# Kernel tuning notes

Measured on AMD Instinct MI355X. Metric: run time of the kernel, lower is better.

## Reference

```python
import jax, jax.numpy as jnp
import numpy as np
import math

SCALE = 30.0
OUT_INDICATOR = 1.0  # easy_margin=False -> out_indicator = 1


def setup_inputs() -> dict:
    key = jax.random.key(0)
    k1, k2, k3 = jax.random.split(key, 3)
    B, D, C = 1024, 512, 100000
    feat = jax.random.normal(k1, (B, D), dtype=jnp.float32)
    label = jax.random.randint(k2, (B,), 0, C, dtype=jnp.int64)
    # xavier_uniform_ init for weights [C, D]
    limit = math.sqrt(6.0 / (C + D))
    weights = jax.random.uniform(k3, (C, D), dtype=jnp.float32, minval=-limit, maxval=limit)
    return {"feat": feat, "label": label, "weights": weights}


def reference(feat, label, weights):
    # L2-normalize features and class weights
    norm_f = jnp.linalg.norm(feat, axis=-1, keepdims=True)        # [B,1]
    nf = feat / norm_f
    norm_w = jnp.linalg.norm(weights, axis=-1, keepdims=True)     # [C,1]
    nw = weights / norm_w
    cos = nf @ nw.T                                               # [B,C]

    avg_w_norm = jnp.mean(norm_w)
    avg_x_norm = jnp.mean(norm_f)

    B = feat.shape[0]
    idx = jnp.arange(B)
    target_cos = jnp.clip(cos[idx, label], -1.0, 1.0)             # [B]
    thetas = jnp.arccos(target_cos) / jnp.pi * 180.0              # degrees, [B]

    max_theta = jnp.max(thetas)
    min_theta = jnp.min(thetas)
    avg_theta = jnp.mean(thetas)
    stdv_theta = jnp.std(thetas, ddof=1)                          # sample stddev (n-1)

    # per-sample dynamic margin (radians). In the torch code these are Python
    # floats computed via .item(), hence constants w.r.t. autograd.
    margin_above = jnp.where(max_theta < 90.0, (90.0 - avg_theta) / 180.0 * jnp.pi, 0.0)
    margin_below = min_theta / 180.0 * jnp.pi
    the_margin = jnp.where(thetas > avg_theta, margin_above, margin_below)  # [B]

    in_range = target_cos > -jnp.cos(the_margin)
    margin_add = jnp.where(in_range, the_margin, 0.0)
    margin_ext = jnp.where(in_range, 0.0, -the_margin * jnp.sin(the_margin)) * OUT_INDICATOR
    margin_add = jax.lax.stop_gradient(margin_add)
    margin_ext = jax.lax.stop_gradient(margin_ext)

    # cos(acos(cos) + margin) only differs from cos at target positions
    target_marginal = jnp.cos(jnp.arccos(target_cos) + margin_add) + margin_ext  # [B]
    marginal_logits = SCALE * cos.at[idx, label].set(target_marginal)            # [B,C]

    return (cos, marginal_logits, avg_theta, min_theta, max_theta,
            stdv_theta, avg_w_norm, avg_x_norm)
```

## Files before the change

kernel.cpp:

```cpp
#include <hip/hip_runtime.h>
#include <math.h>
#include <stdint.h>


typedef _Float16 f16x8 __attribute__((ext_vector_type(8)));
typedef float f32x4 __attribute__((ext_vector_type(4)));

#define SCALE_S 30.0f
#define RAD2DEG 57.29577951308232f
#define DEG2RAD 0.017453292519943295f

#define GL16(g, l)                                                    \
  __builtin_amdgcn_global_load_lds(                                   \
      (const __attribute__((address_space(1))) void*)(g),             \
      (__attribute__((address_space(3))) void*)(l), 16, 0, 0)

__global__ __launch_bounds__(64) void norm_cvt_kernel(
    const float* __restrict__ X, _Float16* __restrict__ X16, int K, int Cn,
    float* __restrict__ nrm, float* __restrict__ inv) {
  const int row = blockIdx.x;
  const int t = threadIdx.x;
  _Float16* o = X16 + (size_t)row * K;
  if (row >= Cn) {
    for (int k = t * 8; k < K; k += 64 * 8)
      *(f16x8*)(o + k) = (f16x8)(_Float16)0.f;
    return;
  }
  const float* r = X + (size_t)row * K;
  float s = 0.f;
  for (int k = t * 8; k < K; k += 64 * 8) {
    float4 v0 = *(const float4*)(r + k);
    float4 v1 = *(const float4*)(r + k + 4);
    s += v0.x * v0.x + v0.y * v0.y + v0.z * v0.z + v0.w * v0.w +
         v1.x * v1.x + v1.y * v1.y + v1.z * v1.z + v1.w * v1.w;
    f16x8 h;
    h[0] = (_Float16)v0.x; h[1] = (_Float16)v0.y;
    h[2] = (_Float16)v0.z; h[3] = (_Float16)v0.w;
    h[4] = (_Float16)v1.x; h[5] = (_Float16)v1.y;
    h[6] = (_Float16)v1.z; h[7] = (_Float16)v1.w;
    *(f16x8*)(o + k) = h;
  }
#pragma unroll
  for (int off = 32; off > 0; off >>= 1) s += __shfl_down(s, off);
  if (t == 0) {
    float n = sqrtf(s);
    nrm[row] = n;
    inv[row] = 1.0f / n;
  }
}

__global__ __launch_bounds__(64) void row_norms_kernel(
    const float* __restrict__ X, int K,
    float* __restrict__ nrm, float* __restrict__ inv) {
  const int row = blockIdx.x;
  const float* r = X + (size_t)row * K;
  const int t = threadIdx.x;
  float s = 0.f;
  for (int k = t * 4; k < K; k += 64 * 4) {
    float4 v = *(const float4*)(r + k);
    s += v.x * v.x + v.y * v.y + v.z * v.z + v.w * v.w;
  }
#pragma unroll
  for (int off = 32; off > 0; off >>= 1) s += __shfl_down(s, off);
  if (t == 0) {
    float n = sqrtf(s);
    nrm[row] = n;
    inv[row] = 1.0f / n;
  }
}

__global__ __launch_bounds__(256) void gemm_cos_lds(
    const _Float16* __restrict__ A16, const _Float16* __restrict__ W16,
    const float* __restrict__ inv_nf, const float* __restrict__ inv_nw,
    float* __restrict__ cosO, float* __restrict__ margO,
    int Cn, int npanel) {
  __shared__ __align__(16) _Float16 Ash[128 * 64];
  __shared__ __align__(16) _Float16 Wsh[128 * 64];
  const int K = 512;

  const int nblk = npanel * 8;
  const int lin = blockIdx.x;
  const int q = nblk >> 3;
  const int wg = (lin & 7) * q + (lin >> 3);
  const int bm = (wg & 7) * 128;
  const int bn = (wg >> 3) * 128;

  const int t = threadIdx.x;
  const int lane = t & 63;
  const int w = t >> 6;
  const int wm = (w >> 1) * 64;
  const int wn = (w & 1) * 64;
  const int lrow = lane >> 4;
  const int lcol = lane & 15;

  const _Float16* srcA[4];
  const _Float16* srcW[4];
  _Float16* dstA[4];
  _Float16* dstW[4];
#pragma unroll
  for (int i = 0; i < 4; ++i) {
    const int slot = w * 4 + i;
    const int c = slot * 64 + lane;
    const int row = c >> 3;
    const int kc = (c & 7) ^ (row & 7);
    srcA[i] = A16 + (size_t)(bm + row) * K + kc * 8;
    srcW[i] = W16 + (size_t)(bn + row) * K + kc * 8;
    dstA[i] = Ash + slot * 512;
    dstW[i] = Wsh + slot * 512;
  }

  f32x4 acc[4][4];
#pragma unroll
  for (int m = 0; m < 4; ++m)
#pragma unroll
    for (int n = 0; n < 4; ++n) acc[m][n] = (f32x4)0.f;

  for (int s = 0; s < 8; ++s) {
    __syncthreads();
#pragma unroll
    for (int i = 0; i < 4; ++i) {
      GL16(srcA[i], dstA[i]);
      GL16(srcW[i], dstW[i]);
      srcA[i] += 64;
      srcW[i] += 64;
    }
    __syncthreads();

#pragma unroll
    for (int ks = 0; ks < 2; ++ks) {
      f16x8 af[4], bf[4];
      const int kc = ks * 4 + lrow;
#pragma unroll
      for (int m = 0; m < 4; ++m) {
        const int rowa = wm + m * 16 + lcol;
        af[m] = *(const f16x8*)(Ash + rowa * 64 + ((kc ^ (rowa & 7)) * 8));
        const int rowb = wn + m * 16 + lcol;
        bf[m] = *(const f16x8*)(Wsh + rowb * 64 + ((kc ^ (rowb & 7)) * 8));
      }
#pragma unroll
      for (int m = 0; m < 4; ++m)
#pragma unroll
        for (int n = 0; n < 4; ++n)
          acc[m][n] = __builtin_amdgcn_mfma_f32_16x16x32_f16(
              af[m], bf[n], acc[m][n], 0, 0, 0);
    }
  }

  float fi[4][4];
#pragma unroll
  for (int m = 0; m < 4; ++m)
#pragma unroll
    for (int r = 0; r < 4; ++r)
      fi[m][r] = inv_nf[bm + wm + m * 16 + lrow * 4 + r];

#pragma unroll
  for (int n = 0; n < 4; ++n) {
    const int col = bn + wn + n * 16 + lcol;
    if (col < Cn) {
      const float wiv = inv_nw[col];
#pragma unroll
      for (int m = 0; m < 4; ++m) {
        const int row0 = bm + wm + m * 16 + lrow * 4;
#pragma unroll
        for (int r = 0; r < 4; ++r) {
          const float v = acc[m][n][r] * fi[m][r] * wiv;
          const size_t o = (size_t)(row0 + r) * Cn + col;
          __builtin_nontemporal_store(v, cosO + o);
          __builtin_nontemporal_store(SCALE_S * v, margO + o);
        }
      }
    }
  }
}

__global__ __launch_bounds__(256) void gemm_cos_f16(
    const float* __restrict__ A, const float* __restrict__ W,
    const float* __restrict__ inv_nf, const float* __restrict__ inv_nw,
    float* __restrict__ cosO, float* __restrict__ margO,
    int Cn, int K, int npanel) {
  __shared__ __align__(16) _Float16 Ash[128 * 64];
  __shared__ __align__(16) _Float16 Wsh[128 * 64];

  const int nblk = npanel * 8;
  const int lin = blockIdx.x;
  const int q = nblk >> 3;
  const int wg = (lin & 7) * q + (lin >> 3);
  const int bm = (wg & 7) * 128;
  const int bn = (wg >> 3) * 128;

  const int t = threadIdx.x;
  const int lane = t & 63;
  const int wid = t >> 6;
  const int wm = (wid >> 1) * 64;
  const int wn = (wid & 1) * 64;
  const int lrow = lane >> 4;
  const int lcol = lane & 15;

  int srow[4], skc[4];
#pragma unroll
  for (int j = 0; j < 4; ++j) {
    const int c = t + 256 * j;
    srow[j] = c >> 3;
    skc[j] = (t & 7) ^ (srow[j] & 7);
  }

  f32x4 acc[4][4];
#pragma unroll
  for (int m = 0; m < 4; ++m)
#pragma unroll
    for (int n = 0; n < 4; ++n) acc[m][n] = (f32x4)0.f;

  float4 ra[4][2], rw[4][2];
#pragma unroll
  for (int j = 0; j < 4; ++j) {
    const float* ap = A + (size_t)(bm + srow[j]) * K + skc[j] * 8;
    ra[j][0] = *(const float4*)ap;
    ra[j][1] = *(const float4*)(ap + 4);
    const int wr = bn + srow[j];
    if (wr < Cn) {
      const float* wp = W + (size_t)wr * K + skc[j] * 8;
      rw[j][0] = *(const float4*)wp;
      rw[j][1] = *(const float4*)(wp + 4);
    } else {
      rw[j][0] = make_float4(0.f, 0.f, 0.f, 0.f);
      rw[j][1] = make_float4(0.f, 0.f, 0.f, 0.f);
    }
  }

  const int nstep = K / 64;
  for (int s = 0; s < nstep; ++s) {
    __syncthreads();
#pragma unroll
    for (int j = 0; j < 4; ++j) {
      const int c = t + 256 * j;
      f16x8 ha, hw;
#pragma unroll
      for (int qq = 0; qq < 4; ++qq) {
        ha[qq] = (_Float16)((&ra[j][0].x)[qq]);
        ha[4 + qq] = (_Float16)((&ra[j][1].x)[qq]);
        hw[qq] = (_Float16)((&rw[j][0].x)[qq]);
        hw[4 + qq] = (_Float16)((&rw[j][1].x)[qq]);
      }
      *(f16x8*)(Ash + c * 8) = ha;
      *(f16x8*)(Wsh + c * 8) = hw;
    }
    __syncthreads();

    if (s + 1 < nstep) {
      const int k0 = (s + 1) * 64;
#pragma unroll
      for (int j = 0; j < 4; ++j) {
        const float* ap = A + (size_t)(bm + srow[j]) * K + k0 + skc[j] * 8;
        ra[j][0] = *(const float4*)ap;
        ra[j][1] = *(const float4*)(ap + 4);
        const int wr = bn + srow[j];
        if (wr < Cn) {
          const float* wp = W + (size_t)wr * K + k0 + skc[j] * 8;
          rw[j][0] = *(const float4*)wp;
          rw[j][1] = *(const float4*)(wp + 4);
        } else {
          rw[j][0] = make_float4(0.f, 0.f, 0.f, 0.f);
          rw[j][1] = make_float4(0.f, 0.f, 0.f, 0.f);
        }
      }
    }

#pragma unroll
    for (int ks = 0; ks < 2; ++ks) {
      f16x8 af[4], bf[4];
      const int kc = ks * 4 + lrow;
#pragma unroll
      for (int m = 0; m < 4; ++m) {
        const int rowa = wm + m * 16 + lcol;
        af[m] = *(const f16x8*)(Ash + rowa * 64 + ((kc ^ (rowa & 7)) * 8));
        const int rowb = wn + m * 16 + lcol;
        bf[m] = *(const f16x8*)(Wsh + rowb * 64 + ((kc ^ (rowb & 7)) * 8));
      }
#pragma unroll
      for (int m = 0; m < 4; ++m)
#pragma unroll
        for (int n = 0; n < 4; ++n)
          acc[m][n] = __builtin_amdgcn_mfma_f32_16x16x32_f16(
              af[m], bf[n], acc[m][n], 0, 0, 0);
    }
  }

  float fi[4][4];
#pragma unroll
  for (int m = 0; m < 4; ++m)
#pragma unroll
    for (int r = 0; r < 4; ++r)
      fi[m][r] = inv_nf[bm + wm + m * 16 + lrow * 4 + r];

#pragma unroll
  for (int n = 0; n < 4; ++n) {
    const int col = bn + wn + n * 16 + lcol;
    if (col < Cn) {
      const float wiv = inv_nw[col];
#pragma unroll
      for (int m = 0; m < 4; ++m) {
        const int row0 = bm + wm + m * 16 + lrow * 4;
#pragma unroll
        for (int r = 0; r < 4; ++r) {
          const float v = acc[m][n][r] * fi[m][r] * wiv;
          const size_t o = (size_t)(row0 + r) * Cn + col;
          __builtin_nontemporal_store(v, cosO + o);
          __builtin_nontemporal_store(SCALE_S * v, margO + o);
        }
      }
    }
  }
}

__global__ __launch_bounds__(1024) void stats_fixup_kernel(
    const float* __restrict__ cosO, float* __restrict__ margO,
    const int* __restrict__ label,
    const float* __restrict__ norm_f, const float* __restrict__ norm_w,
    float* __restrict__ scal, int B, int Cn, int Wn) {
  __shared__ float red[1024];
  __shared__ float s_stat[4];
  const int t = threadIdx.x;

  const int lb = label[t];
  float tc = cosO[(size_t)t * Cn + lb];
  tc = fminf(1.0f, fmaxf(-1.0f, tc));
  const float theta = acosf(tc) * RAD2DEG;

  red[t] = theta; __syncthreads();
  for (int s = 512; s > 0; s >>= 1) {
    if (t < s) red[t] += red[t + s];
    __syncthreads();
  }
  if (t == 0) s_stat[2] = red[0] / (float)B;
  __syncthreads();
  const float avg = s_stat[2];
  __syncthreads();

  red[t] = theta; __syncthreads();
  for (int s = 512; s > 0; s >>= 1) {
    if (t < s) red[t] = fmaxf(red[t], red[t + s]);
    __syncthreads();
  }
  if (t == 0) s_stat[0] = red[0];
  __syncthreads();
  const float mx = s_stat[0];
  __syncthreads();

  red[t] = theta; __syncthreads();
  for (int s = 512; s > 0; s >>= 1) {
    if (t < s) red[t] = fminf(red[t], red[t + s]);
    __syncthreads();
  }
  if (t == 0) s_stat[1] = red[0];
  __syncthreads();
  const float mn = s_stat[1];
  __syncthreads();

  {
    const float d = theta - avg;
    red[t] = d * d;
  }
  __syncthreads();
  for (int s = 512; s > 0; s >>= 1) {
    if (t < s) red[t] += red[t + s];
    __syncthreads();
  }
  const float stdv = sqrtf(red[0] / (float)(B - 1));
  __syncthreads();

  const float margin_above = (mx < 90.0f) ? (90.0f - avg) * DEG2RAD : 0.0f;
  const float margin_below = mn * DEG2RAD;
  const float the_margin = (theta > avg) ? margin_above : margin_below;
  const bool in_range = tc > -cosf(the_margin);
  const float margin_add = in_range ? the_margin : 0.0f;
  const float margin_ext = in_range ? 0.0f : -the_margin * sinf(the_margin);
  const float tmarg = cosf(acosf(tc) + margin_add) + margin_ext;
  margO[(size_t)t * Cn + lb] = SCALE_S * tmarg;

  float pw = 0.f;
  for (int i = t; i < Wn; i += 1024) pw += norm_w[i];
  red[t] = pw; __syncthreads();
  for (int s = 512; s > 0; s >>= 1) {
    if (t < s) red[t] += red[t + s];
    __syncthreads();
  }
  const float avg_w = red[0] / (float)Wn;
  __syncthreads();

  red[t] = norm_f[t]; __syncthreads();
  for (int s = 512; s > 0; s >>= 1) {
    if (t < s) red[t] += red[t + s];
    __syncthreads();
  }
  const float avg_x = red[0] / (float)B;

  if (t == 0) {
    scal[0] = avg;
    scal[1] = mn;
    scal[2] = mx;
    scal[3] = stdv;
    scal[4] = avg_w;
    scal[5] = avg_x;
  }
}

extern "C" void kernel_launch(void* const* d_in, const int* in_sizes, int n_in,
                              void* d_out, int out_size, void* d_ws, size_t ws_size,
                              hipStream_t stream) {
  const float* feat = (const float*)d_in[0];
  const int* label = (const int*)d_in[1];
  const float* W = (const float*)d_in[2];

  const int B = in_sizes[1];
  const int K = in_sizes[0] / B;
  const int Cn = in_sizes[2] / K;
  const int CnPad = ((Cn + 127) / 128) * 128;
  const int npanel = CnPad / 128;

  float* cosO = (float*)d_out;
  float* margO = cosO + (size_t)B * Cn;
  float* scal = margO + (size_t)B * Cn;

  float* norm_f = (float*)d_ws;
  float* inv_nf = norm_f + B;
  float* norm_w = inv_nf + B;
  float* inv_nw = norm_w + CnPad;
  _Float16* A16 = (_Float16*)(inv_nw + CnPad);
  _Float16* W16 = A16 + (size_t)B * K;

  const size_t need = sizeof(float) * (2 * (size_t)B + 2 * (size_t)CnPad) +
                      sizeof(_Float16) * ((size_t)B * K + (size_t)CnPad * K);

  if (ws_size >= need) {
    norm_cvt_kernel<<<B, 64, 0, stream>>>(feat, A16, K, B, norm_f, inv_nf);
    norm_cvt_kernel<<<CnPad, 64, 0, stream>>>(W, W16, K, Cn, norm_w, inv_nw);
    gemm_cos_lds<<<npanel * 8, 256, 0, stream>>>(A16, W16, inv_nf, inv_nw,
                                                 cosO, margO, Cn, npanel);
  } else {
    row_norms_kernel<<<B, 64, 0, stream>>>(feat, K, norm_f, inv_nf);
    row_norms_kernel<<<Cn, 64, 0, stream>>>(W, K, norm_w, inv_nw);
    gemm_cos_f16<<<npanel * 8, 256, 0, stream>>>(feat, W, inv_nf, inv_nw,
                                                 cosO, margO, Cn, K, npanel);
  }

  stats_fixup_kernel<<<1, B, 0, stream>>>(cosO, margO, label, norm_f, norm_w,
                                          scal, B, Cn, Cn);
}
```

Measured before the change: 371.7 us.

## Double-buffer GEMM LDS tiles and pack four rows per norm-convert block

The GEMM now keeps two LDS buffers for the A and W tiles. It prefetches the next K-slab with global_load_lds while computing on the current one, which drops one barrier per iteration and overlaps load latency with MFMA work. The norm/convert kernel now handles four rows per 256-thread block and uses nontemporal loads and stores to avoid polluting the cache with the streamed weights. Double buffering doubles LDS use per block, which may reduce occupancy, and the fast path now also requires K to be a multiple of 512.

```diff
diff --git a/kernel.cpp b/kernel.cpp
--- a/kernel.cpp
+++ b/kernel.cpp
@@ -15,22 +15,31 @@
       (const __attribute__((address_space(1))) void*)(g),             \
       (__attribute__((address_space(3))) void*)(l), 16, 0, 0)
 
-__global__ __launch_bounds__(64) void norm_cvt_kernel(
+__global__ __launch_bounds__(256) void norm_cvt4(
     const float* __restrict__ X, _Float16* __restrict__ X16, int K, int Cn,
-    float* __restrict__ nrm, float* __restrict__ inv) {
-  const int row = blockIdx.x;
-  const int t = threadIdx.x;
+    float* __restrict__ nrm, float* __restrict__ inv, int rows) {
+  const int wid = threadIdx.x >> 6;
+  const int lane = threadIdx.x & 63;
+  const int row = blockIdx.x * 4 + wid;
+  if (row >= rows) return;
   _Float16* o = X16 + (size_t)row * K;
   if (row >= Cn) {
-    for (int k = t * 8; k < K; k += 64 * 8)
-      *(f16x8*)(o + k) = (f16x8)(_Float16)0.f;
+    for (int k = lane * 8; k < K; k += 512)
+      __builtin_nontemporal_store((f16x8)(_Float16)0.f, (f16x8*)(o + k));
     return;
   }
   const float* r = X + (size_t)row * K;
   float s = 0.f;
-  for (int k = t * 8; k < K; k += 64 * 8) {
-    float4 v0 = *(const float4*)(r + k);
-    float4 v1 = *(const float4*)(r + k + 4);
+  for (int k = lane * 8; k < K; k += 512) {
+    float4 v0, v1;
+    v0.x = __builtin_nontemporal_load(r + k + 0);
+    v0.y = __builtin_nontemporal_load(r + k + 1);
+    v0.z = __builtin_nontemporal_load(r + k + 2);
+    v0.w = __builtin_nontemporal_load(r + k + 3);
+    v1.x = __builtin_nontemporal_load(r + k + 4);
+    v1.y = __builtin_nontemporal_load(r + k + 5);
+    v1.z = __builtin_nontemporal_load(r + k + 6);
+    v1.w = __builtin_nontemporal_load(r + k + 7);
     s += v0.x * v0.x + v0.y * v0.y + v0.z * v0.z + v0.w * v0.w +
          v1.x * v1.x + v1.y * v1.y + v1.z * v1.z + v1.w * v1.w;
     f16x8 h;
@@ -38,11 +47,11 @@
     h[2] = (_Float16)v0.z; h[3] = (_Float16)v0.w;
     h[4] = (_Float16)v1.x; h[5] = (_Float16)v1.y;
     h[6] = (_Float16)v1.z; h[7] = (_Float16)v1.w;
-    *(f16x8*)(o + k) = h;
+    __builtin_nontemporal_store(h, (f16x8*)(o + k));
   }
 #pragma unroll
   for (int off = 32; off > 0; off >>= 1) s += __shfl_down(s, off);
-  if (t == 0) {
+  if (lane == 0) {
     float n = sqrtf(s);
     nrm[row] = n;
     inv[row] = 1.0f / n;
@@ -74,8 +83,8 @@
     const float* __restrict__ inv_nf, const float* __restrict__ inv_nw,
     float* __restrict__ cosO, float* __restrict__ margO,
     int Cn, int npanel) {
-  __shared__ __align__(16) _Float16 Ash[128 * 64];
-  __shared__ __align__(16) _Float16 Wsh[128 * 64];
+  __shared__ __align__(16) _Float16 Ash[2][128 * 64];
+  __shared__ __align__(16) _Float16 Wsh[2][128 * 64];
   const int K = 512;
 
   const int nblk = npanel * 8;
@@ -88,6 +97,7 @@
   const int t = threadIdx.x;
   const int lane = t & 63;
   const int w = t >> 6;
+  const int w4 = w * 4;
   const int wm = (w >> 1) * 64;
   const int wn = (w & 1) * 64;
   const int lrow = lane >> 4;
@@ -95,18 +105,13 @@
 
   const _Float16* srcA[4];
   const _Float16* srcW[4];
-  _Float16* dstA[4];
-  _Float16* dstW[4];
 #pragma unroll
   for (int i = 0; i < 4; ++i) {
-    const int slot = w * 4 + i;
-    const int c = slot * 64 + lane;
+    const int c = (w4 + i) * 64 + lane;
     const int row = c >> 3;
     const int kc = (c & 7) ^ (row & 7);
     srcA[i] = A16 + (size_t)(bm + row) * K + kc * 8;
     srcW[i] = W16 + (size_t)(bn + row) * K + kc * 8;
-    dstA[i] = Ash + slot * 512;
-    dstW[i] = Wsh + slot * 512;
   }
 
   f32x4 acc[4][4];
@@ -115,17 +120,27 @@
 #pragma unroll
     for (int n = 0; n < 4; ++n) acc[m][n] = (f32x4)0.f;
 
+#pragma unroll
+  for (int i = 0; i < 4; ++i) {
+    GL16(srcA[i], &Ash[0][(w4 + i) * 512]);
+    GL16(srcW[i], &Wsh[0][(w4 + i) * 512]);
+    srcA[i] += 64;
+    srcW[i] += 64;
+  }
+
+#pragma unroll
   for (int s = 0; s < 8; ++s) {
-    __syncthreads();
-#pragma unroll
-    for (int i = 0; i < 4; ++i) {
-      GL16(srcA[i], dstA[i]);
-      GL16(srcW[i], dstW[i]);
-      srcA[i] += 64;
-      srcW[i] += 64;
-    }
-    __syncthreads();
-
+    const int cur = s & 1;
+    __syncthreads();
+    if (s < 7) {
+#pragma unroll
+      for (int i = 0; i < 4; ++i) {
+        GL16(srcA[i], &Ash[cur ^ 1][(w4 + i) * 512]);
+        GL16(srcW[i], &Wsh[cur ^ 1][(w4 + i) * 512]);
+        srcA[i] += 64;
+        srcW[i] += 64;
+      }
+    }
 #pragma unroll
     for (int ks = 0; ks < 2; ++ks) {
       f16x8 af[4], bf[4];
@@ -133,9 +148,9 @@
 #pragma unroll
       for (int m = 0; m < 4; ++m) {
         const int rowa = wm + m * 16 + lcol;
-        af[m] = *(const f16x8*)(Ash + rowa * 64 + ((kc ^ (rowa & 7)) * 8));
+        af[m] = *(const f16x8*)(&Ash[cur][rowa * 64 + ((kc ^ (rowa & 7)) * 8)]);
         const int rowb = wn + m * 16 + lcol;
-        bf[m] = *(const f16x8*)(Wsh + rowb * 64 + ((kc ^ (rowb & 7)) * 8));
+        bf[m] = *(const f16x8*)(&Wsh[cur][rowb * 64 + ((kc ^ (rowb & 7)) * 8)]);
       }
 #pragma unroll
       for (int m = 0; m < 4; ++m)
@@ -431,9 +446,10 @@
   const size_t need = sizeof(float) * (2 * (size_t)B + 2 * (size_t)CnPad) +
                       sizeof(_Float16) * ((size_t)B * K + (size_t)CnPad * K);
 
-  if (ws_size >= need) {
-    norm_cvt_kernel<<<B, 64, 0, stream>>>(feat, A16, K, B, norm_f, inv_nf);
-    norm_cvt_kernel<<<CnPad, 64, 0, stream>>>(W, W16, K, Cn, norm_w, inv_nw);
+  if (ws_size >= need && (K % 512) == 0) {
+    norm_cvt4<<<B / 4, 256, 0, stream>>>(feat, A16, K, B, norm_f, inv_nf, B);
+    norm_cvt4<<<CnPad / 4, 256, 0, stream>>>(W, W16, K, Cn, norm_w, inv_nw,
+                                             CnPad);
     gemm_cos_lds<<<npanel * 8, 256, 0, stream>>>(A16, W16, inv_nf, inv_nw,
                                                  cosO, margO, Cn, npanel);
   } else {
```

Result: slower. 575.4 us (+54.8%).

## Double-buffer GEMM LDS tiles with K=32 stages and vectorize norm sum

Applied to the files above, without the earlier changes.

The cosine GEMM now splits K into sixteen 32-wide stages held in two LDS buffers. The next stage's global-to-LDS loads are issued before the current stage's MFMAs, so load latency can overlap compute and one barrier per stage is removed. The XOR swizzle is rewritten for the narrower 32-element rows. The weight-norm average in the fixup kernel now reads four floats per load, and the fast path is guarded on K being a multiple of 512. Each stage has half the MFMA work per barrier, and the new swizzle may cause LDS bank conflicts.

```diff
diff --git a/kernel.cpp b/kernel.cpp
--- a/kernel.cpp
+++ b/kernel.cpp
@@ -74,8 +74,8 @@
     const float* __restrict__ inv_nf, const float* __restrict__ inv_nw,
     float* __restrict__ cosO, float* __restrict__ margO,
     int Cn, int npanel) {
-  __shared__ __align__(16) _Float16 Ash[128 * 64];
-  __shared__ __align__(16) _Float16 Wsh[128 * 64];
+  __shared__ __align__(16) _Float16 Ash[2][128 * 32];
+  __shared__ __align__(16) _Float16 Wsh[2][128 * 32];
   const int K = 512;
 
   const int nblk = npanel * 8;
@@ -93,20 +93,15 @@
   const int lrow = lane >> 4;
   const int lcol = lane & 15;
 
-  const _Float16* srcA[4];
-  const _Float16* srcW[4];
-  _Float16* dstA[4];
-  _Float16* dstW[4];
-#pragma unroll
-  for (int i = 0; i < 4; ++i) {
-    const int slot = w * 4 + i;
-    const int c = slot * 64 + lane;
-    const int row = c >> 3;
-    const int kc = (c & 7) ^ (row & 7);
-    srcA[i] = A16 + (size_t)(bm + row) * K + kc * 8;
-    srcW[i] = W16 + (size_t)(bn + row) * K + kc * 8;
-    dstA[i] = Ash + slot * 512;
-    dstW[i] = Wsh + slot * 512;
+  const _Float16* srcA[2];
+  const _Float16* srcW[2];
+#pragma unroll
+  for (int i = 0; i < 2; ++i) {
+    const int c = (w * 2 + i) * 64 + lane;
+    const int row = c >> 2;
+    const int kcs = (c & 3) ^ ((row >> 1) & 3);
+    srcA[i] = A16 + (size_t)(bm + row) * K + kcs * 8;
+    srcW[i] = W16 + (size_t)(bn + row) * K + kcs * 8;
   }
 
   f32x4 acc[4][4];
@@ -115,35 +110,41 @@
 #pragma unroll
     for (int n = 0; n < 4; ++n) acc[m][n] = (f32x4)0.f;
 
-  for (int s = 0; s < 8; ++s) {
-    __syncthreads();
-#pragma unroll
-    for (int i = 0; i < 4; ++i) {
-      GL16(srcA[i], dstA[i]);
-      GL16(srcW[i], dstW[i]);
-      srcA[i] += 64;
-      srcW[i] += 64;
-    }
-    __syncthreads();
-
-#pragma unroll
-    for (int ks = 0; ks < 2; ++ks) {
-      f16x8 af[4], bf[4];
-      const int kc = ks * 4 + lrow;
-#pragma unroll
-      for (int m = 0; m < 4; ++m) {
-        const int rowa = wm + m * 16 + lcol;
-        af[m] = *(const f16x8*)(Ash + rowa * 64 + ((kc ^ (rowa & 7)) * 8));
-        const int rowb = wn + m * 16 + lcol;
-        bf[m] = *(const f16x8*)(Wsh + rowb * 64 + ((kc ^ (rowb & 7)) * 8));
-      }
-#pragma unroll
-      for (int m = 0; m < 4; ++m)
-#pragma unroll
-        for (int n = 0; n < 4; ++n)
-          acc[m][n] = __builtin_amdgcn_mfma_f32_16x16x32_f16(
-              af[m], bf[n], acc[m][n], 0, 0, 0);
-    }
+#pragma unroll
+  for (int i = 0; i < 2; ++i) {
+    GL16(srcA[i], &Ash[0][(w * 2 + i) * 512]);
+    GL16(srcW[i], &Wsh[0][(w * 2 + i) * 512]);
+    srcA[i] += 32;
+    srcW[i] += 32;
+  }
+  __syncthreads();
+
+  for (int s = 0; s < 16; ++s) {
+    const int cur = s & 1;
+    if (s < 15) {
+#pragma unroll
+      for (int i = 0; i < 2; ++i) {
+        GL16(srcA[i], &Ash[cur ^ 1][(w * 2 + i) * 512]);
+        GL16(srcW[i], &Wsh[cur ^ 1][(w * 2 + i) * 512]);
+        srcA[i] += 32;
+        srcW[i] += 32;
+      }
+    }
+    f16x8 af[4], bf[4];
+#pragma unroll
+    for (int m = 0; m < 4; ++m) {
+      const int rowa = wm + m * 16 + lcol;
+      af[m] = *(const f16x8*)(&Ash[cur][rowa * 32 + ((lrow ^ ((rowa >> 1) & 3)) * 8)]);
+      const int rowb = wn + m * 16 + lcol;
+      bf[m] = *(const f16x8*)(&Wsh[cur][rowb * 32 + ((lrow ^ ((rowb >> 1) & 3)) * 8)]);
+    }
+#pragma unroll
+    for (int m = 0; m < 4; ++m)
+#pragma unroll
+      for (int n = 0; n < 4; ++n)
+        acc[m][n] = __builtin_amdgcn_mfma_f32_16x16x32_f16(
+            af[m], bf[n], acc[m][n], 0, 0, 0);
+    __syncthreads();
   }
 
   float fi[4][4];
@@ -378,7 +379,14 @@
   margO[(size_t)t * Cn + lb] = SCALE_S * tmarg;
 
   float pw = 0.f;
-  for (int i = t; i < Wn; i += 1024) pw += norm_w[i];
+  if ((Wn & 3) == 0) {
+    for (int i = t * 4; i < Wn; i += 4096) {
+      f32x4 v = *(const f32x4*)(norm_w + i);
+      pw += v[0] + v[1] + v[2] + v[3];
+    }
+  } else {
+    for (int i = t; i < Wn; i += 1024) pw += norm_w[i];
+  }
   red[t] = pw; __syncthreads();
   for (int s = 512; s > 0; s >>= 1) {
     if (t < s) red[t] += red[t + s];
@@ -431,7 +439,7 @@
   const size_t need = sizeof(float) * (2 * (size_t)B + 2 * (size_t)CnPad) +
                       sizeof(_Float16) * ((size_t)B * K + (size_t)CnPad * K);
 
-  if (ws_size >= need) {
+  if (ws_size >= need && (K % 512) == 0) {
     norm_cvt_kernel<<<B, 64, 0, stream>>>(feat, A16, K, B, norm_f, inv_nf);
     norm_cvt_kernel<<<CnPad, 64, 0, stream>>>(W, W16, K, Cn, norm_w, inv_nw);
     gemm_cos_lds<<<npanel * 8, 256, 0, stream>>>(A16, W16, inv_nf, inv_nw,
```

After: 382.9 us. 1.03x slower.
